# Kernel optimization log

Measured on AMD Instinct MI355X. Metric: run time of the kernel, lower is better.

Reference implementation:

```python
import jax, jax.numpy as jnp
import numpy as np

N_QUBITS = 4
N_LAYERS = 2
_I2 = jnp.eye(2, dtype=jnp.complex64)
_X = jnp.array([[0.0, 1.0], [1.0, 0.0]], dtype=jnp.complex64)


def _apply_1q_batched(state, U, wire):
    # state: [B,2,2,2,2] complex, U: [B,2,2] (per-sample gate)
    s = jnp.moveaxis(state, 1 + wire, -1)
    s = jnp.einsum('bij,b...j->b...i', U, s)
    return jnp.moveaxis(s, -1, 1 + wire)


def _apply_1q(state, U, wire):
    # shared 2x2 gate on `wire`
    s = jnp.moveaxis(state, 1 + wire, -1)
    s = jnp.einsum('ij,...j->...i', U, s)
    return jnp.moveaxis(s, -1, 1 + wire)


def _apply_cnot(state, c, t):
    s = jnp.moveaxis(state, (1 + c, 1 + t), (-2, -1))  # [...,2(ctrl),2(tgt)]
    s = jnp.stack([s[..., 0, :], s[..., 1, ::-1]], axis=-2)  # flip target if ctrl=1
    return jnp.moveaxis(s, (-2, -1), (1 + c, 1 + t))


def _rot_matrix(phi, theta, omega):
    # qml.Rot = RZ(omega) @ RY(theta) @ RZ(phi)
    c, s = jnp.cos(theta / 2), jnp.sin(theta / 2)
    ep = jnp.exp(-0.5j * (phi + omega))  # e^{-i(phi+omega)/2}
    em = jnp.exp(-0.5j * (phi - omega))  # e^{-i(phi-omega)/2}
    return jnp.stack([
        jnp.stack([ep * c, -jnp.conj(em) * s]),
        jnp.stack([em * s, jnp.conj(ep) * c]),
    ]).astype(jnp.complex64)


def _circuit(angles, weights):
    # angles: [B, 4] real; weights: [2, 4, 3] real -> [B, 4] PauliZ expvals
    B = angles.shape[0]
    state = jnp.zeros((B,) + (2,) * N_QUBITS, jnp.complex64)
    state = state.at[(slice(None),) + (0,) * N_QUBITS].set(1.0)  # |0000>
    # AngleEmbedding (rotation='X'): RX(angle_w) on wire w, batched over samples
    for w in range(N_QUBITS):
        half = angles[:, w] / 2
        c, s = jnp.cos(half), jnp.sin(half)
        U = c[:, None, None] * _I2 - 1j * s[:, None, None] * _X  # [B,2,2]
        state = _apply_1q_batched(state, U, w)
    # StronglyEntanglingLayers: Rot on each wire, then ring of CNOTs with range r
    for l in range(N_LAYERS):
        for w in range(N_QUBITS):
            U = _rot_matrix(weights[l, w, 0], weights[l, w, 1], weights[l, w, 2])
            state = _apply_1q(state, U, w)
        r = (l % (N_QUBITS - 1)) + 1  # PennyLane default ranges
        for w in range(N_QUBITS):
            state = _apply_cnot(state, w, (w + r) % N_QUBITS)
    probs = state.real ** 2 + state.imag ** 2  # [B,2,2,2,2]
    z = []
    for w in range(N_QUBITS):
        other = tuple(a for a in range(1, N_QUBITS + 1) if a != 1 + w)
        p = probs.sum(other)  # [B,2]
        z.append(p[:, 0] - p[:, 1])
    return jnp.stack(z, axis=-1)  # [B,4]


def setup_inputs() -> dict:
    key = jax.random.key(0)
    ks = jax.random.split(key, 6)
    B, D_IN, D_OUT, NQ = 65536, 512, 512, N_QUBITS
    x = jax.random.normal(ks[0], (B, D_IN), jnp.float32)
    pre_W = jax.random.normal(ks[1], (NQ, D_IN), jnp.float32) / np.sqrt(D_IN)
    pre_b = jax.random.normal(ks[2], (NQ,), jnp.float32) * 0.05
    weights = jax.random.uniform(ks[3], (N_LAYERS, NQ, 3), jnp.float32) * (2 * np.pi)
    post_W = jax.random.normal(ks[4], (D_OUT, NQ), jnp.float32) / np.sqrt(NQ)
    post_b = jax.random.normal(ks[5], (D_OUT,), jnp.float32) * 0.05
    return {"x": x, "pre_W": pre_W, "pre_b": pre_b, "weights": weights,
            "post_W": post_W, "post_b": post_b}


def reference(x, pre_W, pre_b, weights, post_W, post_b):
    angles = jnp.tanh(x @ pre_W.T + pre_b) * jnp.pi  # [B,4]
    q = _circuit(angles, weights)                    # [B,4]
    return q @ post_W.T + post_b                     # [B,512]
```

## Files before the change

### kernel.cpp

```cpp
#include <hip/hip_runtime.h>
#include <math.h>

#define PI_F 3.14159265358979323846f


typedef float floatx4 __attribute__((ext_vector_type(4)));

static __device__ __forceinline__ void nt_store4(float* p, floatx4 v)
{
    __builtin_nontemporal_store(v, reinterpret_cast<floatx4*>(p));
}

static __device__ __forceinline__ float fast_tanh(float a)
{
    a = fminf(fmaxf(a, -15.f), 15.f);
    const float e = __expf(2.f * a);
    return (e - 1.f) / (e + 1.f);
}

__global__ __launch_bounds__(256) void k_angles(
    const float* __restrict__ x,
    const float* __restrict__ preW,
    const float* __restrict__ preb,
    float* __restrict__ abase, int astride, int B)
{
    const int lane = threadIdx.x & 63;
    const int wid  = (blockIdx.x * blockDim.x + threadIdx.x) >> 6;
    const int b0   = wid * 4;
    if (b0 >= B) return;

    float4 wA[4], wB[4];
#pragma unroll
    for (int w = 0; w < 4; ++w) {
        wA[w] = *reinterpret_cast<const float4*>(preW + w * 512 + lane * 4);
        wB[w] = *reinterpret_cast<const float4*>(preW + w * 512 + 256 + lane * 4);
    }
    const float4 pb = *reinterpret_cast<const float4*>(preb);

    float acc[4][4];
#pragma unroll
    for (int t = 0; t < 4; ++t) {
        const float* xr = x + (size_t)(b0 + t) * 512;
        const float4 xa = *reinterpret_cast<const float4*>(xr + lane * 4);
        const float4 xb = *reinterpret_cast<const float4*>(xr + 256 + lane * 4);
#pragma unroll
        for (int w = 0; w < 4; ++w) {
            acc[t][w] = xa.x * wA[w].x + xa.y * wA[w].y + xa.z * wA[w].z + xa.w * wA[w].w
                      + xb.x * wB[w].x + xb.y * wB[w].y + xb.z * wB[w].z + xb.w * wB[w].w;
        }
    }

    float v[4];
#pragma unroll
    for (int t = 0; t < 4; ++t) {
        float a01 = (lane & 1) ? acc[t][1] : acc[t][0];
        float b01 = (lane & 1) ? acc[t][0] : acc[t][1];
        a01 += __shfl_xor(b01, 1, 64);
        float a23 = (lane & 1) ? acc[t][3] : acc[t][2];
        float b23 = (lane & 1) ? acc[t][2] : acc[t][3];
        a23 += __shfl_xor(b23, 1, 64);
        const float vv = (lane & 2) ? a23 : a01;
        const float uu = (lane & 2) ? a01 : a23;
        v[t] = vv + __shfl_xor(uu, 2, 64);
    }
    float c01 = (lane & 4) ? v[1] : v[0];
    float d01 = (lane & 4) ? v[0] : v[1];
    c01 += __shfl_xor(d01, 4, 64);
    float c23 = (lane & 4) ? v[3] : v[2];
    float d23 = (lane & 4) ? v[2] : v[3];
    c23 += __shfl_xor(d23, 4, 64);
    float m = (lane & 8) ? c23 : c01;
    float n = (lane & 8) ? c01 : c23;
    m += __shfl_xor(n, 8, 64);
    m += __shfl_xor(m, 16, 64);
    m += __shfl_xor(m, 32, 64);

    const float pb01 = (lane & 1) ? pb.y : pb.x;
    const float pb23 = (lane & 1) ? pb.w : pb.z;
    const float pbv  = (lane & 2) ? pb23 : pb01;
    const float angv = fast_tanh(m + pbv) * PI_F;

    if (lane < 16)
        abase[(size_t)(b0 + (lane >> 2)) * astride + (lane & 3)] = angv;
}

template<int WIRE>
__device__ __forceinline__ void apply1q(float* sr, float* si,
    float u00r, float u00i, float u01r, float u01i,
    float u10r, float u10i, float u11r, float u11i)
{
    constexpr int st = 1 << (3 - WIRE);
#pragma unroll
    for (int i = 0; i < 16; ++i) {
        if (i & st) continue;
        const int j = i | st;
        const float r0 = sr[i], m0 = si[i], r1 = sr[j], m1 = si[j];
        sr[i] = u00r * r0 - u00i * m0 + u01r * r1 - u01i * m1;
        si[i] = u00r * m0 + u00i * r0 + u01r * m1 + u01i * r1;
        sr[j] = u10r * r0 - u10i * m0 + u11r * r1 - u11i * m1;
        si[j] = u10r * m0 + u10i * r0 + u11r * m1 + u11i * r1;
    }
}

template<int CW, int TW>
__device__ __forceinline__ void cnot(float* sr, float* si)
{
    constexpr int cb = 1 << (3 - CW), tb = 1 << (3 - TW);
#pragma unroll
    for (int i = 0; i < 16; ++i) {
        if ((i & cb) && !(i & tb)) {
            const int j = i | tb;
            float t;
            t = sr[i]; sr[i] = sr[j]; sr[j] = t;
            t = si[i]; si[i] = si[j]; si[j] = t;
        }
    }
}

#define APPLY_FAST(L, W) { \
    const float ph = wts[((L) * 4 + (W)) * 3 + 0]; \
    const float th = wts[((L) * 4 + (W)) * 3 + 1]; \
    const float om = wts[((L) * 4 + (W)) * 3 + 2]; \
    const float s_  = __sinf(0.5f * th),        c_  = __cosf(0.5f * th); \
    const float sp_ = __sinf(0.5f * (ph + om)), cp_ = __cosf(0.5f * (ph + om)); \
    const float sq_ = __sinf(0.5f * (ph - om)), cq_ = __cosf(0.5f * (ph - om)); \
    apply1q<W>(sr, si, cp_ * c_, -sp_ * c_, -cq_ * s_, -sq_ * s_, \
                       cq_ * s_, -sq_ * s_, cp_ * c_,  sp_ * c_); }

__global__ __launch_bounds__(256) void k_circuit_out(
    const float* abase, int astride,
    const float* __restrict__ wts,
    const float* __restrict__ postW,
    const float* __restrict__ postb,
    float* out, int B)
{
    const int lane = threadIdx.x & 63;
    const int wv   = (blockIdx.x * blockDim.x + threadIdx.x) >> 6;
    const int b0   = wv * 16;
    if (b0 >= B) return;
    const int sid  = lane >> 2;
    const int b    = b0 + sid;

    const float4 ang = *reinterpret_cast<const float4*>(abase + (size_t)b * astride);

    const float s0 = __sinf(0.5f * ang.x), c0 = __cosf(0.5f * ang.x);
    const float s1 = __sinf(0.5f * ang.y), c1 = __cosf(0.5f * ang.y);
    const float s2 = __sinf(0.5f * ang.z), c2 = __cosf(0.5f * ang.z);
    const float s3 = __sinf(0.5f * ang.w), c3 = __cosf(0.5f * ang.w);

    float sr[16], si[16];
#pragma unroll
    for (int i = 0; i < 16; ++i) {
        const float r = ((i & 8) ? s0 : c0) * ((i & 4) ? s1 : c1)
                      * ((i & 2) ? s2 : c2) * ((i & 1) ? s3 : c3);
        const int mm = (((i >> 3) & 1) + ((i >> 2) & 1) + ((i >> 1) & 1) + (i & 1)) & 3;
        switch (mm) {
            case 0:  sr[i] = r;    si[i] = 0.f; break;
            case 1:  sr[i] = 0.f;  si[i] = -r;  break;
            case 2:  sr[i] = -r;   si[i] = 0.f; break;
            default: sr[i] = 0.f;  si[i] = r;   break;
        }
    }

    APPLY_FAST(0, 0); APPLY_FAST(0, 1); APPLY_FAST(0, 2); APPLY_FAST(0, 3);
    cnot<0, 1>(sr, si); cnot<1, 2>(sr, si); cnot<2, 3>(sr, si); cnot<3, 0>(sr, si);
    APPLY_FAST(1, 0); APPLY_FAST(1, 1); APPLY_FAST(1, 2); APPLY_FAST(1, 3);
    cnot<0, 2>(sr, si); cnot<1, 3>(sr, si); cnot<2, 0>(sr, si); cnot<3, 1>(sr, si);

    float z0 = 0.f, z1 = 0.f, z2 = 0.f, z3 = 0.f;
#pragma unroll
    for (int i = 0; i < 16; ++i) {
        const float p = sr[i] * sr[i] + si[i] * si[i];
        z0 += (i & 8) ? -p : p;
        z1 += (i & 4) ? -p : p;
        z2 += (i & 2) ? -p : p;
        z3 += (i & 1) ? -p : p;
    }

    const float4* pW4 = reinterpret_cast<const float4*>(postW);
    const float4* pb4 = reinterpret_cast<const float4*>(postb);
    const float4 p0 = pW4[4 * lane + 0], p1 = pW4[4 * lane + 1];
    const float4 p2 = pW4[4 * lane + 2], p3 = pW4[4 * lane + 3];
    const float4 p4 = pW4[4 * (64 + lane) + 0], p5 = pW4[4 * (64 + lane) + 1];
    const float4 p6 = pW4[4 * (64 + lane) + 2], p7 = pW4[4 * (64 + lane) + 3];
    const float4 bb0 = pb4[lane], bb1 = pb4[64 + lane];

#pragma unroll
    for (int s = 0; s < 16; ++s) {
        const float q0 = __shfl(z0, s * 4, 64);
        const float q1 = __shfl(z1, s * 4, 64);
        const float q2 = __shfl(z2, s * 4, 64);
        const float q3 = __shfl(z3, s * 4, 64);
        floatx4 o0, o1;
        o0.x = fmaf(q3, p0.w, fmaf(q2, p0.z, fmaf(q1, p0.y, fmaf(q0, p0.x, bb0.x))));
        o0.y = fmaf(q3, p1.w, fmaf(q2, p1.z, fmaf(q1, p1.y, fmaf(q0, p1.x, bb0.y))));
        o0.z = fmaf(q3, p2.w, fmaf(q2, p2.z, fmaf(q1, p2.y, fmaf(q0, p2.x, bb0.z))));
        o0.w = fmaf(q3, p3.w, fmaf(q2, p3.z, fmaf(q1, p3.y, fmaf(q0, p3.x, bb0.w))));
        o1.x = fmaf(q3, p4.w, fmaf(q2, p4.z, fmaf(q1, p4.y, fmaf(q0, p4.x, bb1.x))));
        o1.y = fmaf(q3, p5.w, fmaf(q2, p5.z, fmaf(q1, p5.y, fmaf(q0, p5.x, bb1.y))));
        o1.z = fmaf(q3, p6.w, fmaf(q2, p6.z, fmaf(q1, p6.y, fmaf(q0, p6.x, bb1.z))));
        o1.w = fmaf(q3, p7.w, fmaf(q2, p7.z, fmaf(q1, p7.y, fmaf(q0, p7.x, bb1.w))));
        float* orow = out + (size_t)(b0 + s) * 512;
        nt_store4(orow + 4 * lane, o0);
        nt_store4(orow + 256 + 4 * lane, o1);
    }
}

extern "C" void kernel_launch(void* const* d_in, const int* in_sizes, int n_in,
                              void* d_out, int out_size, void* d_ws, size_t ws_size,
                              hipStream_t stream)
{
    const float* x     = (const float*)d_in[0];
    const float* preW  = (const float*)d_in[1];
    const float* preb  = (const float*)d_in[2];
    const float* wts   = (const float*)d_in[3];
    const float* postW = (const float*)d_in[4];
    const float* postb = (const float*)d_in[5];
    float* out = (float*)d_out;
    const int B = in_sizes[0] / 512;

    const size_t angBytes = (size_t)B * 4 * sizeof(float);
    float* abase; int astride;
    if (ws_size >= angBytes) { abase = (float*)d_ws; astride = 4; }
    else { abase = out + 508; astride = 512; }

    k_angles<<<dim3((B + 15) / 16), dim3(256), 0, stream>>>(x, preW, preb, abase, astride, B);
    k_circuit_out<<<dim3(B / 64), dim3(256), 0, stream>>>(abase, astride, wts, postW, postb, out, B);
}
```

Measured before the change: 50.52 us.

## Fuse angle projection, circuit simulation and output projection into one kernel

Merges the two kernels into a single kernel. Each wavefront computes angles for 4 samples, broadcasts them by shuffle to 16-lane groups, simulates the circuit, and writes the 4 output rows. This removes the second launch and the angle round-trip through workspace, and hoists all x loads ahead of the dot products. In exchange, each lane group simulates a redundant copy of the circuit (16 lanes per sample instead of 4), so trig and gate math per output grows fourfold.

```diff
diff --git a/kernel.cpp b/kernel.cpp
--- a/kernel.cpp
+++ b/kernel.cpp
@@ -18,17 +18,70 @@
     return (e - 1.f) / (e + 1.f);
 }
 
-__global__ __launch_bounds__(256) void k_angles(
+template<int WIRE>
+__device__ __forceinline__ void apply1q(float* sr, float* si,
+    float u00r, float u00i, float u01r, float u01i,
+    float u10r, float u10i, float u11r, float u11i)
+{
+    constexpr int st = 1 << (3 - WIRE);
+#pragma unroll
+    for (int i = 0; i < 16; ++i) {
+        if (i & st) continue;
+        const int j = i | st;
+        const float r0 = sr[i], m0 = si[i], r1 = sr[j], m1 = si[j];
+        sr[i] = u00r * r0 - u00i * m0 + u01r * r1 - u01i * m1;
+        si[i] = u00r * m0 + u00i * r0 + u01r * m1 + u01i * r1;
+        sr[j] = u10r * r0 - u10i * m0 + u11r * r1 - u11i * m1;
+        si[j] = u10r * m0 + u10i * r0 + u11r * m1 + u11i * r1;
+    }
+}
+
+template<int CW, int TW>
+__device__ __forceinline__ void cnot(float* sr, float* si)
+{
+    constexpr int cb = 1 << (3 - CW), tb = 1 << (3 - TW);
+#pragma unroll
+    for (int i = 0; i < 16; ++i) {
+        if ((i & cb) && !(i & tb)) {
+            const int j = i | tb;
+            float t;
+            t = sr[i]; sr[i] = sr[j]; sr[j] = t;
+            t = si[i]; si[i] = si[j]; si[j] = t;
+        }
+    }
+}
+
+#define APPLY_FAST(L, W) { \
+    const float ph = wts[((L) * 4 + (W)) * 3 + 0]; \
+    const float th = wts[((L) * 4 + (W)) * 3 + 1]; \
+    const float om = wts[((L) * 4 + (W)) * 3 + 2]; \
+    const float s_  = __sinf(0.5f * th),        c_  = __cosf(0.5f * th); \
+    const float sp_ = __sinf(0.5f * (ph + om)), cp_ = __cosf(0.5f * (ph + om)); \
+    const float sq_ = __sinf(0.5f * (ph - om)), cq_ = __cosf(0.5f * (ph - om)); \
+    apply1q<W>(sr, si, cp_ * c_, -sp_ * c_, -cq_ * s_, -sq_ * s_, \
+                       cq_ * s_, -sq_ * s_, cp_ * c_,  sp_ * c_); }
+
+__global__ __launch_bounds__(256) void k_fused(
     const float* __restrict__ x,
     const float* __restrict__ preW,
     const float* __restrict__ preb,
-    float* __restrict__ abase, int astride, int B)
+    const float* __restrict__ wts,
+    const float* __restrict__ postW,
+    const float* __restrict__ postb,
+    float* __restrict__ out, int B)
 {
     const int lane = threadIdx.x & 63;
-    const int wid  = (blockIdx.x * blockDim.x + threadIdx.x) >> 6;
-    const int b0   = wid * 4;
+    const int wv   = (blockIdx.x * blockDim.x + threadIdx.x) >> 6;
+    const int b0   = wv * 4;
     if (b0 >= B) return;
 
+    float4 xa[4], xb[4];
+#pragma unroll
+    for (int t = 0; t < 4; ++t) {
+        const float* xr = x + (size_t)(b0 + t) * 512;
+        xa[t] = *reinterpret_cast<const float4*>(xr + lane * 4);
+        xb[t] = *reinterpret_cast<const float4*>(xr + 256 + lane * 4);
+    }
     float4 wA[4], wB[4];
 #pragma unroll
     for (int w = 0; w < 4; ++w) {
@@ -40,13 +93,10 @@
     float acc[4][4];
 #pragma unroll
     for (int t = 0; t < 4; ++t) {
-        const float* xr = x + (size_t)(b0 + t) * 512;
-        const float4 xa = *reinterpret_cast<const float4*>(xr + lane * 4);
-        const float4 xb = *reinterpret_cast<const float4*>(xr + 256 + lane * 4);
 #pragma unroll
         for (int w = 0; w < 4; ++w) {
-            acc[t][w] = xa.x * wA[w].x + xa.y * wA[w].y + xa.z * wA[w].z + xa.w * wA[w].w
-                      + xb.x * wB[w].x + xb.y * wB[w].y + xb.z * wB[w].z + xb.w * wB[w].w;
+            acc[t][w] = xa[t].x * wA[w].x + xa[t].y * wA[w].y + xa[t].z * wA[w].z + xa[t].w * wA[w].w
+                      + xb[t].x * wB[w].x + xb[t].y * wB[w].y + xb[t].z * wB[w].z + xb[t].w * wB[w].w;
         }
     }
 
@@ -80,73 +130,16 @@
     const float pbv  = (lane & 2) ? pb23 : pb01;
     const float angv = fast_tanh(m + pbv) * PI_F;
 
-    if (lane < 16)
-        abase[(size_t)(b0 + (lane >> 2)) * astride + (lane & 3)] = angv;
-}
-
-template<int WIRE>
-__device__ __forceinline__ void apply1q(float* sr, float* si,
-    float u00r, float u00i, float u01r, float u01i,
-    float u10r, float u10i, float u11r, float u11i)
-{
-    constexpr int st = 1 << (3 - WIRE);
-#pragma unroll
-    for (int i = 0; i < 16; ++i) {
-        if (i & st) continue;
-        const int j = i | st;
-        const float r0 = sr[i], m0 = si[i], r1 = sr[j], m1 = si[j];
-        sr[i] = u00r * r0 - u00i * m0 + u01r * r1 - u01i * m1;
-        si[i] = u00r * m0 + u00i * r0 + u01r * m1 + u01i * r1;
-        sr[j] = u10r * r0 - u10i * m0 + u11r * r1 - u11i * m1;
-        si[j] = u10r * m0 + u10i * r0 + u11r * m1 + u11i * r1;
-    }
-}
-
-template<int CW, int TW>
-__device__ __forceinline__ void cnot(float* sr, float* si)
-{
-    constexpr int cb = 1 << (3 - CW), tb = 1 << (3 - TW);
-#pragma unroll
-    for (int i = 0; i < 16; ++i) {
-        if ((i & cb) && !(i & tb)) {
-            const int j = i | tb;
-            float t;
-            t = sr[i]; sr[i] = sr[j]; sr[j] = t;
-            t = si[i]; si[i] = si[j]; si[j] = t;
-        }
-    }
-}
-
-#define APPLY_FAST(L, W) { \
-    const float ph = wts[((L) * 4 + (W)) * 3 + 0]; \
-    const float th = wts[((L) * 4 + (W)) * 3 + 1]; \
-    const float om = wts[((L) * 4 + (W)) * 3 + 2]; \
-    const float s_  = __sinf(0.5f * th),        c_  = __cosf(0.5f * th); \
-    const float sp_ = __sinf(0.5f * (ph + om)), cp_ = __cosf(0.5f * (ph + om)); \
-    const float sq_ = __sinf(0.5f * (ph - om)), cq_ = __cosf(0.5f * (ph - om)); \
-    apply1q<W>(sr, si, cp_ * c_, -sp_ * c_, -cq_ * s_, -sq_ * s_, \
-                       cq_ * s_, -sq_ * s_, cp_ * c_,  sp_ * c_); }
-
-__global__ __launch_bounds__(256) void k_circuit_out(
-    const float* abase, int astride,
-    const float* __restrict__ wts,
-    const float* __restrict__ postW,
-    const float* __restrict__ postb,
-    float* out, int B)
-{
-    const int lane = threadIdx.x & 63;
-    const int wv   = (blockIdx.x * blockDim.x + threadIdx.x) >> 6;
-    const int b0   = wv * 16;
-    if (b0 >= B) return;
-    const int sid  = lane >> 2;
-    const int b    = b0 + sid;
-
-    const float4 ang = *reinterpret_cast<const float4*>(abase + (size_t)b * astride);
-
-    const float s0 = __sinf(0.5f * ang.x), c0 = __cosf(0.5f * ang.x);
-    const float s1 = __sinf(0.5f * ang.y), c1 = __cosf(0.5f * ang.y);
-    const float s2 = __sinf(0.5f * ang.z), c2 = __cosf(0.5f * ang.z);
-    const float s3 = __sinf(0.5f * ang.w), c3 = __cosf(0.5f * ang.w);
+    const int t16 = lane >> 4;
+    const float a0 = __shfl(angv, t16 * 4 + 0, 64);
+    const float a1 = __shfl(angv, t16 * 4 + 1, 64);
+    const float a2 = __shfl(angv, t16 * 4 + 2, 64);
+    const float a3 = __shfl(angv, t16 * 4 + 3, 64);
+
+    const float s0 = __sinf(0.5f * a0), c0 = __cosf(0.5f * a0);
+    const float s1 = __sinf(0.5f * a1), c1 = __cosf(0.5f * a1);
+    const float s2 = __sinf(0.5f * a2), c2 = __cosf(0.5f * a2);
+    const float s3 = __sinf(0.5f * a3), c3 = __cosf(0.5f * a3);
 
     float sr[16], si[16];
 #pragma unroll
@@ -186,11 +179,11 @@
     const float4 bb0 = pb4[lane], bb1 = pb4[64 + lane];
 
 #pragma unroll
-    for (int s = 0; s < 16; ++s) {
-        const float q0 = __shfl(z0, s * 4, 64);
-        const float q1 = __shfl(z1, s * 4, 64);
-        const float q2 = __shfl(z2, s * 4, 64);
-        const float q3 = __shfl(z3, s * 4, 64);
+    for (int s = 0; s < 4; ++s) {
+        const float q0 = __shfl(z0, s * 16, 64);
+        const float q1 = __shfl(z1, s * 16, 64);
+        const float q2 = __shfl(z2, s * 16, 64);
+        const float q3 = __shfl(z3, s * 16, 64);
         floatx4 o0, o1;
         o0.x = fmaf(q3, p0.w, fmaf(q2, p0.z, fmaf(q1, p0.y, fmaf(q0, p0.x, bb0.x))));
         o0.y = fmaf(q3, p1.w, fmaf(q2, p1.z, fmaf(q1, p1.y, fmaf(q0, p1.x, bb0.y))));
@@ -219,11 +212,6 @@
     float* out = (float*)d_out;
     const int B = in_sizes[0] / 512;
 
-    const size_t angBytes = (size_t)B * 4 * sizeof(float);
-    float* abase; int astride;
-    if (ws_size >= angBytes) { abase = (float*)d_ws; astride = 4; }
-    else { abase = out + 508; astride = 512; }
-
-    k_angles<<<dim3((B + 15) / 16), dim3(256), 0, stream>>>(x, preW, preb, abase, astride, B);
-    k_circuit_out<<<dim3(B / 64), dim3(256), 0, stream>>>(abase, astride, wts, postW, postb, out, B);
-}
+    k_fused<<<dim3((B + 15) / 16), dim3(256), 0, stream>>>(
+        x, preW, preb, wts, postW, postb, out, B);
+}
```

Measured after the change: 70.85 us. +40.2%, slower.
